# Optimization experiments

Hardware: AMD Instinct MI355X
Metric: run time of the kernel (lower is better)

Reference implementation:

```python
import jax, jax.numpy as jnp
from jax import lax
import numpy as np

CONF = 0.5        # config.video.detection_confidence
MAX_FACES = 8     # config.video.max_faces
EPS = 1e-5        # BatchNorm eps (inference mode: running stats)


def setup_inputs() -> dict:
    key = jax.random.key(0)
    ks = jax.random.split(key, 8)
    def w(k, shape):
        return jax.random.normal(k, shape, jnp.float32) * 0.05
    B, H, W = 32, 512, 512
    f32 = jnp.float32
    return {
        "x": jax.random.normal(ks[0], (B, 3, H, W), f32),
        # backbone conv1 (3->32, s2) + BN
        "w1": w(ks[1], (32, 3, 3, 3)), "b1": jnp.zeros(32, f32),
        "g1": jnp.ones(32, f32), "be1": jnp.zeros(32, f32),
        "m1": jnp.zeros(32, f32), "v1": jnp.ones(32, f32),
        # backbone conv2 (32->64, s2) + BN
        "w2": w(ks[2], (64, 32, 3, 3)), "b2": jnp.zeros(64, f32),
        "g2": jnp.ones(64, f32), "be2": jnp.zeros(64, f32),
        "m2": jnp.zeros(64, f32), "v2": jnp.ones(64, f32),
        # backbone conv3 (64->128, s2) + BN
        "w3": w(ks[3], (128, 64, 3, 3)), "b3": jnp.zeros(128, f32),
        "g3": jnp.ones(128, f32), "be3": jnp.zeros(128, f32),
        "m3": jnp.zeros(128, f32), "v3": jnp.ones(128, f32),
        # detection head (128->256 k3, 256->1 k1)
        "dw1": w(ks[4], (256, 128, 3, 3)), "db1": jnp.zeros(256, f32),
        "dw2": w(ks[5], (1, 256, 1, 1)), "db2": jnp.zeros(1, f32),
        # bbox head (128->256 k3, 256->4 k1)
        "bw1": w(ks[6], (256, 128, 3, 3)), "bb1": jnp.zeros(256, f32),
        "bw2": w(ks[7], (4, 256, 1, 1)), "bb2": jnp.zeros(4, f32),
    }


def _conv(x, w, b, stride, pad):
    y = lax.conv_general_dilated(x, w, (stride, stride), ((pad, pad), (pad, pad)),
                                 dimension_numbers=("NCHW", "OIHW", "NCHW"))
    return y + b[None, :, None, None]


def _bn(x, g, b, m, v):
    scale = (g * lax.rsqrt(v + EPS))[None, :, None, None]
    return (x - m[None, :, None, None]) * scale + b[None, :, None, None]


def reference(x, w1, b1, g1, be1, m1, v1, w2, b2, g2, be2, m2, v2,
              w3, b3, g3, be3, m3, v3, dw1, db1, dw2, db2, bw1, bb1, bw2, bb2):
    h = jax.nn.relu(_bn(_conv(x, w1, b1, 2, 1), g1, be1, m1, v1))
    h = jax.nn.relu(_bn(_conv(h, w2, b2, 2, 1), g2, be2, m2, v2))
    h = jax.nn.relu(_bn(_conv(h, w3, b3, 2, 1), g3, be3, m3, v3))
    # heads
    det = jax.nn.sigmoid(_conv(jax.nn.relu(_conv(h, dw1, db1, 1, 1)), dw2, db2, 1, 0))[:, 0]  # [B,Hf,Wf]
    bbox = _conv(jax.nn.relu(_conv(h, bw1, bb1, 1, 1)), bw2, bb2, 1, 0)  # [B,4,Hf,Wf]
    # fused threshold + top-k + gather (fixed-size, jit-friendly version of the per-image loop)
    B = det.shape[0]
    scores = det.reshape(B, -1)                      # [B, Hf*Wf]
    top_s, top_i = lax.top_k(scores, MAX_FACES)      # [B, K]
    bflat = bbox.reshape(B, 4, -1)                   # [B, 4, Hf*Wf]
    sel = jnp.take_along_axis(bflat, top_i[:, None, :], axis=2)  # [B, 4, K]
    boxes = jax.nn.sigmoid(jnp.swapaxes(sel, 1, 2)) * x.shape[-1]  # [B, K, 4]
    mask = (top_s > CONF)[:, :, None]                # below-threshold slots -> zeros
    return jnp.where(mask, boxes, jnp.zeros((), boxes.dtype))
```

## Files before the change

kernel.cpp:

```cpp
#include <hip/hip_runtime.h>
#include <math.h>

#define EPSBN 1e-5f

typedef __attribute__((ext_vector_type(4))) float f32x4;
typedef __attribute__((ext_vector_type(8))) short s16x8;

__device__ __forceinline__ unsigned short f2bf(float f) {
    unsigned u = __builtin_bit_cast(unsigned, f);
    u = (u + 0x7fffu + ((u >> 16) & 1u)) >> 16;
    return (unsigned short)u;
}
__device__ __forceinline__ float bf2f(unsigned short s) {
    unsigned u = ((unsigned)s) << 16;
    return __builtin_bit_cast(float, u);
}


__global__ __launch_bounds__(256) void prep_k(
    const float* __restrict__ w1, const float* __restrict__ b1, const float* __restrict__ g1,
    const float* __restrict__ be1, const float* __restrict__ m1, const float* __restrict__ v1,
    const float* __restrict__ w2, const float* __restrict__ b2, const float* __restrict__ g2,
    const float* __restrict__ be2, const float* __restrict__ m2, const float* __restrict__ v2,
    const float* __restrict__ w3, const float* __restrict__ b3, const float* __restrict__ g3,
    const float* __restrict__ be3, const float* __restrict__ m3, const float* __restrict__ v3,
    float* __restrict__ W)
{
    int i = blockIdx.x * 256 + threadIdx.x;
    if (i < 864) {
        int co = i & 31; int r = i >> 5; int ci = r % 3; int kk = r / 3;
        float A = g1[co] * rsqrtf(v1[co] + EPSBN);
        W[i] = w1[(co*3 + ci)*9 + kk] * A;
    } else if (i < 896) {
        int co = i - 864;
        float A = g1[co] * rsqrtf(v1[co] + EPSBN);
        W[i] = (b1[co] - m1[co]) * A + be1[co];
    } else if (i >= 19328 && i < 19392) {
        int co = i - 19328;
        float A = g2[co] * rsqrtf(v2[co] + EPSBN);
        W[i] = (b2[co] - m2[co]) * A + be2[co];
    } else if (i >= 93120 && i < 93248) {
        int co = i - 93120;
        float A = g3[co] * rsqrtf(v3[co] + EPSBN);
        W[i] = (b3[co] - m3[co]) * A + be3[co];
    }
}

__global__ __launch_bounds__(256) void prep2_k(
    const float* __restrict__ dw1, const float* __restrict__ bw1,
    unsigned short* __restrict__ WF)
{
    int i = blockIdx.x * 256 + threadIdx.x;
    if (i >= 1179648) return;
    int head = i / 589824;
    int r    = i - head * 589824;
    int kk   = r >> 16;
    int r2   = r & 65535;
    int cig  = r2 >> 14;
    int pl   = (r2 >> 13) & 1;
    int nf   = (r2 >> 9) & 15;
    int lane = (r2 >> 3) & 63;
    int j    = r2 & 7;
    int ci = cig*32 + (lane >> 4)*8 + j;
    int co = (lane & 15) + nf*16;
    const float* src = head ? bw1 : dw1;
    float w = src[(co*128 + ci)*9 + kk];
    unsigned short h = f2bf(w);
    WF[i] = pl ? f2bf(w - bf2f(h)) : h;
}

__global__ __launch_bounds__(256) void prep3_k(
    const float* __restrict__ w3, const float* __restrict__ g3, const float* __restrict__ v3,
    unsigned short* __restrict__ W3F)
{
    int i = blockIdx.x * 256 + threadIdx.x;
    if (i >= 147456) return;
    int kk = i >> 14;
    int r  = i & 16383;
    int cig = r >> 13;
    int pl  = (r >> 12) & 1;
    int nf  = (r >> 9) & 7;
    int lane = (r >> 3) & 63;
    int j   = r & 7;
    int ci = cig*32 + (lane >> 4)*8 + j;
    int co = nf*16 + (lane & 15);
    float A = g3[co] * rsqrtf(v3[co] + EPSBN);
    float w = w3[(co*64 + ci)*9 + kk] * A;
    unsigned short h = f2bf(w);
    W3F[i] = pl ? f2bf(w - bf2f(h)) : h;
}

__global__ __launch_bounds__(256) void prep4_k(
    const float* __restrict__ w2, const float* __restrict__ g2, const float* __restrict__ v2,
    unsigned short* __restrict__ W2F)
{
    int i = blockIdx.x * 256 + threadIdx.x;
    if (i >= 36864) return;
    int kk = i >> 12;
    int r  = i & 4095;
    int pl  = r >> 11;
    int nfg = (r >> 9) & 3;
    int lane = (r >> 3) & 63;
    int j   = r & 7;
    int ci = (lane >> 4)*8 + j;
    int co = nfg*16 + (lane & 15);
    float A = g2[co] * rsqrtf(v2[co] + EPSBN);
    float w = w2[(co*32 + ci)*9 + kk] * A;
    unsigned short h = f2bf(w);
    W2F[i] = pl ? f2bf(w - bf2f(h)) : h;
}

__global__ __launch_bounds__(256, 4) void conv12mm_k(
    const float* __restrict__ x, const float* __restrict__ W,
    const unsigned short* __restrict__ W2F,
    unsigned short* __restrict__ A2H, unsigned short* __restrict__ A2L, int b0)
{
    __shared__ __attribute__((aligned(16))) unsigned short Ah[9792];
    __shared__ __attribute__((aligned(16))) unsigned short Al[9792];

    const int tid  = threadIdx.x;
    const int lane = tid & 63;
    const int wv   = tid >> 6;
    const int m    = lane & 15;
    const int ks   = lane >> 4;

    const int bl   = blockIdx.x >> 8;
    const int tile = blockIdx.x & 255;
    const int OY = (tile >> 3) * 4;
    const int OX = (tile & 7) * 16;
    const int base1y = 2*OY - 1, base1x = 2*OX - 1;

    const float* xb = x + (size_t)(b0 + bl) * 3 * 262144;

    for (int t = tid; t < 297; t += 256) {
        int row = t / 33, lx = t - row*33;
        int y1 = base1y + row, x1 = base1x + lx;
        float c1[32];
        #pragma unroll
        for (int c = 0; c < 32; c++) c1[c] = 0.f;
        if (((unsigned)y1 < 256u) && ((unsigned)x1 < 256u)) {
            #pragma unroll
            for (int ky = 0; ky < 3; ky++) {
                int xy = 2*y1 + ky - 1;
                if ((unsigned)xy < 512u) {
                    #pragma unroll
                    for (int kx = 0; kx < 3; kx++) {
                        int xx = 2*x1 + kx - 1;
                        if ((unsigned)xx < 512u) {
                            int kk = ky*3 + kx;
                            #pragma unroll
                            for (int ci = 0; ci < 3; ci++) {
                                float v = xb[(size_t)ci*262144 + xy*512 + xx];
                                const float4* w4 = (const float4*)(W + (kk*3+ci)*32);
                                float4 wa = w4[0], wb = w4[1], wc = w4[2], wd = w4[3];
                                float4 we = w4[4], wf = w4[5], wg = w4[6], wh = w4[7];
                                c1[0]  = fmaf(v, wa.x, c1[0]);  c1[1]  = fmaf(v, wa.y, c1[1]);
                                c1[2]  = fmaf(v, wa.z, c1[2]);  c1[3]  = fmaf(v, wa.w, c1[3]);
                                c1[4]  = fmaf(v, wb.x, c1[4]);  c1[5]  = fmaf(v, wb.y, c1[5]);
                                c1[6]  = fmaf(v, wb.z, c1[6]);  c1[7]  = fmaf(v, wb.w, c1[7]);
                                c1[8]  = fmaf(v, wc.x, c1[8]);  c1[9]  = fmaf(v, wc.y, c1[9]);
                                c1[10] = fmaf(v, wc.z, c1[10]); c1[11] = fmaf(v, wc.w, c1[11]);
                                c1[12] = fmaf(v, wd.x, c1[12]); c1[13] = fmaf(v, wd.y, c1[13]);
                                c1[14] = fmaf(v, wd.z, c1[14]); c1[15] = fmaf(v, wd.w, c1[15]);
                                c1[16] = fmaf(v, we.x, c1[16]); c1[17] = fmaf(v, we.y, c1[17]);
                                c1[18] = fmaf(v, we.z, c1[18]); c1[19] = fmaf(v, we.w, c1[19]);
                                c1[20] = fmaf(v, wf.x, c1[20]); c1[21] = fmaf(v, wf.y, c1[21]);
                                c1[22] = fmaf(v, wf.z, c1[22]); c1[23] = fmaf(v, wf.w, c1[23]);
                                c1[24] = fmaf(v, wg.x, c1[24]); c1[25] = fmaf(v, wg.y, c1[25]);
                                c1[26] = fmaf(v, wg.z, c1[26]); c1[27] = fmaf(v, wg.w, c1[27]);
                                c1[28] = fmaf(v, wh.x, c1[28]); c1[29] = fmaf(v, wh.y, c1[29]);
                                c1[30] = fmaf(v, wh.z, c1[30]); c1[31] = fmaf(v, wh.w, c1[31]);
                            }
                        }
                    }
                }
            }
            #pragma unroll
            for (int c = 0; c < 32; c++)
                c1[c] = fmaxf(c1[c] + W[864 + c], 0.f);
        }
        int xi = (lx & 1)*17 + (lx >> 1);
        #pragma unroll
        for (int kg = 0; kg < 4; kg++) {
            uint4 h, l;
            unsigned hw[4], lw[4];
            #pragma unroll
            for (int q = 0; q < 4; q++) {
                float r0 = c1[kg*8 + 2*q], r1 = c1[kg*8 + 2*q + 1];
                unsigned short h0 = f2bf(r0), h1 = f2bf(r1);
                unsigned short l0 = f2bf(r0 - bf2f(h0)), l1 = f2bf(r1 - bf2f(h1));
                hw[q] = (unsigned)h0 | ((unsigned)h1 << 16);
                lw[q] = (unsigned)l0 | ((unsigned)l1 << 16);
            }
            h.x = hw[0]; h.y = hw[1]; h.z = hw[2]; h.w = hw[3];
            l.x = lw[0]; l.y = lw[1]; l.z = lw[2]; l.w = lw[3];
            int a = ((kg*9 + row)*34 + xi)*8;
            *(uint4*)&Ah[a] = h;
            *(uint4*)&Al[a] = l;
        }
    }
    __syncthreads();

    f32x4 acc[4];
    #pragma unroll
    for (int mf = 0; mf < 4; mf++) { f32x4 z = {0.f,0.f,0.f,0.f}; acc[mf] = z; }

    for (int ky = 0; ky < 3; ky++) {
        for (int kx = 0; kx < 3; kx++) {
            int kk = ky*3 + kx;
            int xib = (kx & 1)*17 + (kx >> 1);
            s16x8 ah[4], al[4];
            #pragma unroll
            for (int mf = 0; mf < 4; mf++) {
                int hy = 2*mf + ky;
                int a = ((ks*9 + hy)*34 + xib + m)*8;
                ah[mf] = *(const s16x8*)&Ah[a];
                al[mf] = *(const s16x8*)&Al[a];
            }
            const unsigned short* wb = W2F + kk*4096;
            s16x8 bh  = *(const s16x8*)(wb + wv*512 + lane*8);
            s16x8 blo = *(const s16x8*)(wb + 2048 + wv*512 + lane*8);
            #pragma unroll
            for (int mf = 0; mf < 4; mf++) {
                acc[mf] = __builtin_amdgcn_mfma_f32_16x16x32_bf16(ah[mf], bh,  acc[mf], 0, 0, 0);
                acc[mf] = __builtin_amdgcn_mfma_f32_16x16x32_bf16(ah[mf], blo, acc[mf], 0, 0, 0);
                acc[mf] = __builtin_amdgcn_mfma_f32_16x16x32_bf16(al[mf], bh,  acc[mf], 0, 0, 0);
            }
        }
    }

    const int co = wv*16 + m;
    const float bv = W[19328 + co];
    #pragma unroll
    for (int mf = 0; mf < 4; mf++) {
        int y = OY + mf;
        #pragma unroll
        for (int r = 0; r < 4; r++) {
            int xo = OX + ks*4 + r;
            float rv = fmaxf(acc[mf][r] + bv, 0.f);
            unsigned short h = f2bf(rv);
            unsigned short l = f2bf(rv - bf2f(h));
            size_t a = ((size_t)(bl*16384 + y*128 + xo))*64 + co;
            A2H[a] = h;
            A2L[a] = l;
        }
    }
}

__global__ __launch_bounds__(256, 2) void conv3mm_k(
    const unsigned short* __restrict__ A2H, const unsigned short* __restrict__ A2L,
    const unsigned short* __restrict__ W3F, const float* __restrict__ bias,
    unsigned* __restrict__ A3P)
{
    const int tid  = threadIdx.x;
    const int lane = tid & 63;
    const int w    = tid >> 6;
    const int bl   = blockIdx.x >> 6;
    const int y    = blockIdx.x & 63;
    const int m    = lane & 15;
    const int ks   = lane >> 4;

    f32x4 acc[4][2];
    #pragma unroll
    for (int mf = 0; mf < 4; mf++)
        #pragma unroll
        for (int nfl = 0; nfl < 2; nfl++) {
            f32x4 z = {0.f, 0.f, 0.f, 0.f};
            acc[mf][nfl] = z;
        }

    const size_t ibase = (size_t)bl * 16384 * 64;

    for (int ky = 0; ky < 3; ky++) {
        int iy = 2*y + ky - 1;
        if ((unsigned)iy >= 128u) continue;
        for (int kx = 0; kx < 3; kx++) {
            int kk = ky*3 + kx;
            #pragma unroll
            for (int cig = 0; cig < 2; cig++) {
                s16x8 ah[4], al[4];
                #pragma unroll
                for (int mf = 0; mf < 4; mf++) {
                    int xo = mf*16 + m;
                    int ix = 2*xo + kx - 1;
                    bool v = ix >= 0;
                    int ixc = v ? ix : 0;
                    size_t a = ibase + ((size_t)iy*128 + ixc)*64 + cig*32 + ks*8;
                    s16x8 zh = {0,0,0,0,0,0,0,0};
                    s16x8 th = *(const s16x8*)(A2H + a);
                    s16x8 tl = *(const s16x8*)(A2L + a);
                    ah[mf] = v ? th : zh;
                    al[mf] = v ? tl : zh;
                }
                const unsigned short* wb = W3F + (kk*2 + cig)*8192;
                #pragma unroll
                for (int nfl = 0; nfl < 2; nfl++) {
                    int nfg = w*2 + nfl;
                    s16x8 bh  = *(const s16x8*)(wb + nfg*512 + lane*8);
                    s16x8 blo = *(const s16x8*)(wb + 4096 + nfg*512 + lane*8);
                    #pragma unroll
                    for (int mf = 0; mf < 4; mf++) {
                        acc[mf][nfl] = __builtin_amdgcn_mfma_f32_16x16x32_bf16(ah[mf], bh,  acc[mf][nfl], 0, 0, 0);
                        acc[mf][nfl] = __builtin_amdgcn_mfma_f32_16x16x32_bf16(ah[mf], blo, acc[mf][nfl], 0, 0, 0);
                        acc[mf][nfl] = __builtin_amdgcn_mfma_f32_16x16x32_bf16(al[mf], bh,  acc[mf][nfl], 0, 0, 0);
                    }
                }
            }
        }
    }

    const size_t obase = ((size_t)(bl*64 + y))*64*128;
    #pragma unroll
    for (int nfl = 0; nfl < 2; nfl++) {
        int co = (w*2 + nfl)*16 + m;
        float bv = bias[co];
        #pragma unroll
        for (int mf = 0; mf < 4; mf++) {
            #pragma unroll
            for (int r = 0; r < 4; r++) {
                float rv = fmaxf(acc[mf][nfl][r] + bv, 0.f);
                unsigned short h = f2bf(rv);
                unsigned short l = f2bf(rv - bf2f(h));
                int xo = mf*16 + ks*4 + r;
                A3P[obase + (size_t)xo*128 + co] = (unsigned)h | ((unsigned)l << 16);
            }
        }
    }
}

__global__ __launch_bounds__(512, 4) void headmm_k(
    const unsigned* __restrict__ A3P, const unsigned short* __restrict__ WF,
    const float* __restrict__ db1, const float* __restrict__ dw2, const float* __restrict__ db2,
    const float* __restrict__ bb1, const float* __restrict__ bw2, const float* __restrict__ bb2,
    float* __restrict__ SC, float* __restrict__ BF, int b0)
{
    __shared__ __attribute__((aligned(16))) unsigned short Ah[6528];
    __shared__ __attribute__((aligned(16))) unsigned short Al[6528];
    __shared__ float red[8][4][64];

    const int tid  = threadIdx.x;
    const int lane = tid & 63;
    const int w    = tid >> 6;
    const int head = blockIdx.y;
    const int imgl = blockIdx.x >> 6;
    const int y    = blockIdx.x & 63;

    f32x4 acc[4][2];
    #pragma unroll
    for (int mf = 0; mf < 4; mf++)
        #pragma unroll
        for (int nf = 0; nf < 2; nf++) {
            f32x4 z = {0.f, 0.f, 0.f, 0.f};
            acc[mf][nf] = z;
        }

    const unsigned* abase = A3P + (size_t)imgl * 64 * 64 * 128;
    const unsigned short* WFh = WF + head * 589824;

    uint4 pva[2], pvb[2];
    #define HM_ISSUE(CIG)                                                          \
        _Pragma("unroll")                                                          \
        for (int it = 0; it < 2; it++) {                                           \
            int t = tid + it*512;                                                  \
            uint4 z4 = {0u,0u,0u,0u};                                              \
            pva[it] = z4; pvb[it] = z4;                                            \
            if (t < 792) {                                                         \
                int kgrp = t & 3; int q = t >> 2;                                  \
                int xi = q % 66;  int row = q / 66;                                \
                int gr = y + row - 1, gx = xi - 1;                                 \
                if (((unsigned)gr < 64u) && ((unsigned)gx < 64u)) {                \
                    const uint4* p = (const uint4*)(abase + ((size_t)gr*64 + gx)*128 \
                                                    + (CIG)*32 + kgrp*8);          \
                    pva[it] = p[0]; pvb[it] = p[1];                                \
                }                                                                  \
            }                                                                      \
        }

    HM_ISSUE(0);
    for (int cig = 0; cig < 4; cig++) {
        __syncthreads();
        #pragma unroll
        for (int it = 0; it < 2; it++) {
            int t = tid + it*512;
            if (t < 792) {
                int kgrp = t & 3; int q = t >> 2;
                int xi = q % 66;  int row = q / 66;
                int a = ((kgrp*3 + row)*68 + xi)*8;
                uint4 va = pva[it], vb = pvb[it];
                uint4 h, l;
                h.x = (va.x & 0xffffu) | (va.y << 16);
                h.y = (va.z & 0xffffu) | (va.w << 16);
                h.z = (vb.x & 0xffffu) | (vb.y << 16);
                h.w = (vb.z & 0xffffu) | (vb.w << 16);
                l.x = (va.x >> 16) | (va.y & 0xffff0000u);
                l.y = (va.z >> 16) | (va.w & 0xffff0000u);
                l.z = (vb.x >> 16) | (vb.y & 0xffff0000u);
                l.w = (vb.z >> 16) | (vb.w & 0xffff0000u);
                *(uint4*)&Ah[a] = h;
                *(uint4*)&Al[a] = l;
            }
        }
        if (cig < 3) { HM_ISSUE(cig + 1); }
        __syncthreads();
        __builtin_amdgcn_s_setprio(1);
        #pragma unroll 1
        for (int kk = 0; kk < 9; kk++) {
            int ky = kk / 3, kx = kk - 3*(kk/3);
            s16x8 ah[4], al[4];
            #pragma unroll
            for (int mf = 0; mf < 4; mf++) {
                int xq = (lane & 15) + 16*mf + kx;
                int a = (((lane >> 4)*3 + ky)*68 + xq)*8;
                ah[mf] = *(const s16x8*)&Ah[a];
                al[mf] = *(const s16x8*)&Al[a];
            }
            const unsigned short* wk = WFh + kk*65536 + cig*16384;
            #pragma unroll
            for (int nf = 0; nf < 2; nf++) {
                int nfg = w*2 + nf;
                s16x8 bh = *(const s16x8*)(wk + nfg*512 + lane*8);
                s16x8 bl = *(const s16x8*)(wk + 8192 + nfg*512 + lane*8);
                #pragma unroll
                for (int mf = 0; mf < 4; mf++) {
                    acc[mf][nf] = __builtin_amdgcn_mfma_f32_16x16x32_bf16(ah[mf], bh, acc[mf][nf], 0, 0, 0);
                    acc[mf][nf] = __builtin_amdgcn_mfma_f32_16x16x32_bf16(ah[mf], bl, acc[mf][nf], 0, 0, 0);
                    acc[mf][nf] = __builtin_amdgcn_mfma_f32_16x16x32_bf16(al[mf], bh, acc[mf][nf], 0, 0, 0);
                }
            }
        }
        __builtin_amdgcn_s_setprio(0);
    }
    #undef HM_ISSUE

    const float* b1p = head ? bb1 : db1;
    const float* w2p = head ? bw2 : dw2;
    const float* b2p = head ? bb2 : db2;
    const int NOUT = head ? 4 : 1;

    #pragma unroll
    for (int nf = 0; nf < 2; nf++) {
        float bv = b1p[(lane & 15) + (w*2 + nf)*16];
        #pragma unroll
        for (int mf = 0; mf < 4; mf++)
            #pragma unroll
            for (int r = 0; r < 4; r++)
                acc[mf][nf][r] = fmaxf(acc[mf][nf][r] + bv, 0.f);
    }

    for (int p = 0; p < NOUT; p++) {
        float wq0 = w2p[p*256 + (lane & 15) + (w*2 + 0)*16];
        float wq1 = w2p[p*256 + (lane & 15) + (w*2 + 1)*16];
        #pragma unroll
        for (int mf = 0; mf < 4; mf++) {
            #pragma unroll
            for (int r = 0; r < 4; r++) {
                float v = acc[mf][0][r]*wq0 + acc[mf][1][r]*wq1;
                v += __shfl_xor(v, 1);
                v += __shfl_xor(v, 2);
                v += __shfl_xor(v, 4);
                v += __shfl_xor(v, 8);
                if ((lane & 15) == 0)
                    red[w][p][mf*16 + (lane >> 4)*4 + r] = v;
            }
        }
    }
    __syncthreads();
    float* outp = head ? BF : SC;
    if (tid < NOUT*64) {
        int p = tid >> 6; int px = tid & 63;
        float v = b2p[p];
        #pragma unroll
        for (int ww = 0; ww < 8; ww++) v += red[ww][p][px];
        outp[((size_t)((b0 + imgl)*NOUT + p))*4096 + y*64 + px] = v;
    }
}

__global__ __launch_bounds__(256) void topk_k(
    const float* __restrict__ scores, const float* __restrict__ bflat,
    float* __restrict__ outp)
{
    __shared__ float sv[4096];
    __shared__ float rv[256];
    __shared__ int   ri[256];
    __shared__ float kv[8];
    __shared__ int   kidx[8];
    int b = blockIdx.x, t = threadIdx.x;
    for (int i = t; i < 4096; i += 256) sv[i] = scores[b*4096 + i];
    __syncthreads();
    for (int k = 0; k < 8; k++) {
        float bv = -INFINITY; int bi = 0x7fffffff;
        for (int i = t; i < 4096; i += 256) {
            float v = sv[i];
            if (v > bv || (v == bv && i < bi)) { bv = v; bi = i; }
        }
        rv[t] = bv; ri[t] = bi;
        __syncthreads();
        for (int s = 128; s > 0; s >>= 1) {
            if (t < s) {
                float v2 = rv[t+s]; int i2 = ri[t+s];
                if (v2 > rv[t] || (v2 == rv[t] && i2 < ri[t])) { rv[t] = v2; ri[t] = i2; }
            }
            __syncthreads();
        }
        if (t == 0) { kv[k] = rv[0]; kidx[k] = ri[0]; sv[ri[0]] = -INFINITY; }
        __syncthreads();
    }
    if (t < 32) {
        int k = t >> 2, c = t & 3;
        int idx = kidx[k];
        float s  = 1.f / (1.f + expf(-kv[k]));
        float lg = bflat[((size_t)(b*4 + c))*4096 + idx];
        float box = 512.f / (1.f + expf(-lg));
        outp[(b*8 + k)*4 + c] = (s > 0.5f) ? box : 0.f;
    }
}

extern "C" void kernel_launch(void* const* d_in, const int* in_sizes, int n_in,
                              void* d_out, int out_size, void* d_ws, size_t ws_size,
                              hipStream_t stream)
{
    const float* x   = (const float*)d_in[0];
    const float* w1  = (const float*)d_in[1];
    const float* b1  = (const float*)d_in[2];
    const float* g1  = (const float*)d_in[3];
    const float* be1 = (const float*)d_in[4];
    const float* m1  = (const float*)d_in[5];
    const float* v1  = (const float*)d_in[6];
    const float* w2  = (const float*)d_in[7];
    const float* b2  = (const float*)d_in[8];
    const float* g2  = (const float*)d_in[9];
    const float* be2 = (const float*)d_in[10];
    const float* m2  = (const float*)d_in[11];
    const float* v2  = (const float*)d_in[12];
    const float* w3  = (const float*)d_in[13];
    const float* b3  = (const float*)d_in[14];
    const float* g3  = (const float*)d_in[15];
    const float* be3 = (const float*)d_in[16];
    const float* m3  = (const float*)d_in[17];
    const float* v3  = (const float*)d_in[18];
    const float* dw1 = (const float*)d_in[19];
    const float* db1 = (const float*)d_in[20];
    const float* dw2 = (const float*)d_in[21];
    const float* db2 = (const float*)d_in[22];
    const float* bw1 = (const float*)d_in[23];
    const float* bb1 = (const float*)d_in[24];
    const float* bw2 = (const float*)d_in[25];
    const float* bb2 = (const float*)d_in[26];

    char*  wsb = (char*)d_ws;
    float*          W   = (float*)wsb;
    unsigned short* WF  = (unsigned short*)(wsb + 372992);
    unsigned short* W3F = (unsigned short*)(wsb + 2732288);
    float*          SC  = (float*)(wsb + 3027200);
    float*          BF  = (float*)(wsb + 3551488);
    unsigned short* A2H = (unsigned short*)(wsb + 5648640);
    unsigned short* A2L = (unsigned short*)(wsb + 22425856);
    unsigned*       A3P = (unsigned*)(wsb + 39203072);
    unsigned short* W2F = (unsigned short*)(wsb + 55980288);
    float* out = (float*)d_out;

    prep_k <<<365, 256, 0, stream>>>(w1,b1,g1,be1,m1,v1, w2,b2,g2,be2,m2,v2,
                                     w3,b3,g3,be3,m3,v3, W);
    prep2_k<<<4608, 256, 0, stream>>>(dw1, bw1, WF);
    prep3_k<<<576, 256, 0, stream>>>(w3, g3, v3, W3F);
    prep4_k<<<144, 256, 0, stream>>>(w2, g2, v2, W2F);

    for (int c = 0; c < 4; c++) {
        conv12mm_k<<<2048, 256, 0, stream>>>(x, W, W2F, A2H, A2L, c*8);
        conv3mm_k <<<512, 256, 0, stream>>>(A2H, A2L, W3F, W + 93120, A3P);
        headmm_k  <<<dim3(512, 2), 512, 0, stream>>>(A3P, WF, db1, dw2, db2, bb1, bw2, bb2,
                                                     SC, BF, c*8);
    }
    topk_k<<<32, 256, 0, stream>>>(SC, BF, out);
}
```

Baseline: 728.5 us.

## Fuse detection and bbox heads into one block to share staged activations

The head kernel now computes both heads in the same block instead of launching a separate grid row per head. The staged activation tile in shared memory and its global loads are reused for both weight sets, halving activation traffic and the split/convert work. In exchange, each thread holds twice the accumulators, launch bounds drop to 2 blocks per CU, and the grid has half as many blocks, lowering occupancy. The LDS row stride is also changed from 3 to 4 rows, which enlarges the shared buffers.

```diff
diff --git a/kernel.cpp b/kernel.cpp
--- a/kernel.cpp
+++ b/kernel.cpp
@@ -328,34 +328,34 @@
     }
 }
 
-__global__ __launch_bounds__(512, 4) void headmm_k(
+__global__ __launch_bounds__(512, 2) void headmm_k(
     const unsigned* __restrict__ A3P, const unsigned short* __restrict__ WF,
     const float* __restrict__ db1, const float* __restrict__ dw2, const float* __restrict__ db2,
     const float* __restrict__ bb1, const float* __restrict__ bw2, const float* __restrict__ bb2,
     float* __restrict__ SC, float* __restrict__ BF, int b0)
 {
-    __shared__ __attribute__((aligned(16))) unsigned short Ah[6528];
-    __shared__ __attribute__((aligned(16))) unsigned short Al[6528];
+    __shared__ __attribute__((aligned(16))) unsigned short Ah[8704];
+    __shared__ __attribute__((aligned(16))) unsigned short Al[8704];
     __shared__ float red[8][4][64];
 
     const int tid  = threadIdx.x;
     const int lane = tid & 63;
     const int w    = tid >> 6;
-    const int head = blockIdx.y;
     const int imgl = blockIdx.x >> 6;
     const int y    = blockIdx.x & 63;
 
-    f32x4 acc[4][2];
+    f32x4 acc[4][2][2];
     #pragma unroll
     for (int mf = 0; mf < 4; mf++)
         #pragma unroll
-        for (int nf = 0; nf < 2; nf++) {
-            f32x4 z = {0.f, 0.f, 0.f, 0.f};
-            acc[mf][nf] = z;
-        }
+        for (int nf = 0; nf < 2; nf++)
+            #pragma unroll
+            for (int h = 0; h < 2; h++) {
+                f32x4 z = {0.f, 0.f, 0.f, 0.f};
+                acc[mf][nf][h] = z;
+            }
 
     const unsigned* abase = A3P + (size_t)imgl * 64 * 64 * 128;
-    const unsigned short* WFh = WF + head * 589824;
 
     uint4 pva[2], pvb[2];
     #define HM_ISSUE(CIG)                                                          \
@@ -385,7 +385,7 @@
             if (t < 792) {
                 int kgrp = t & 3; int q = t >> 2;
                 int xi = q % 66;  int row = q / 66;
-                int a = ((kgrp*3 + row)*68 + xi)*8;
+                int a = ((kgrp*4 + row)*68 + xi)*8;
                 uint4 va = pva[it], vb = pvb[it];
                 uint4 h, l;
                 h.x = (va.x & 0xffffu) | (va.y << 16);
@@ -410,21 +410,24 @@
             #pragma unroll
             for (int mf = 0; mf < 4; mf++) {
                 int xq = (lane & 15) + 16*mf + kx;
-                int a = (((lane >> 4)*3 + ky)*68 + xq)*8;
+                int a = (((lane >> 4)*4 + ky)*68 + xq)*8;
                 ah[mf] = *(const s16x8*)&Ah[a];
                 al[mf] = *(const s16x8*)&Al[a];
             }
-            const unsigned short* wk = WFh + kk*65536 + cig*16384;
-            #pragma unroll
-            for (int nf = 0; nf < 2; nf++) {
-                int nfg = w*2 + nf;
-                s16x8 bh = *(const s16x8*)(wk + nfg*512 + lane*8);
-                s16x8 bl = *(const s16x8*)(wk + 8192 + nfg*512 + lane*8);
+            #pragma unroll
+            for (int h = 0; h < 2; h++) {
+                const unsigned short* wk = WF + h*589824 + kk*65536 + cig*16384;
                 #pragma unroll
-                for (int mf = 0; mf < 4; mf++) {
-                    acc[mf][nf] = __builtin_amdgcn_mfma_f32_16x16x32_bf16(ah[mf], bh, acc[mf][nf], 0, 0, 0);
-                    acc[mf][nf] = __builtin_amdgcn_mfma_f32_16x16x32_bf16(ah[mf], bl, acc[mf][nf], 0, 0, 0);
-                    acc[mf][nf] = __builtin_amdgcn_mfma_f32_16x16x32_bf16(al[mf], bh, acc[mf][nf], 0, 0, 0);
+                for (int nf = 0; nf < 2; nf++) {
+                    int nfg = w*2 + nf;
+                    s16x8 bh = *(const s16x8*)(wk + nfg*512 + lane*8);
+                    s16x8 bl = *(const s16x8*)(wk + 8192 + nfg*512 + lane*8);
+                    #pragma unroll
+                    for (int mf = 0; mf < 4; mf++) {
+                        acc[mf][nf][h] = __builtin_amdgcn_mfma_f32_16x16x32_bf16(ah[mf], bh, acc[mf][nf][h], 0, 0, 0);
+                        acc[mf][nf][h] = __builtin_amdgcn_mfma_f32_16x16x32_bf16(ah[mf], bl, acc[mf][nf][h], 0, 0, 0);
+                        acc[mf][nf][h] = __builtin_amdgcn_mfma_f32_16x16x32_bf16(al[mf], bh, acc[mf][nf][h], 0, 0, 0);
+                    }
                 }
             }
         }
@@ -432,46 +435,50 @@
     }
     #undef HM_ISSUE
 
-    const float* b1p = head ? bb1 : db1;
-    const float* w2p = head ? bw2 : dw2;
-    const float* b2p = head ? bb2 : db2;
-    const int NOUT = head ? 4 : 1;
-
-    #pragma unroll
-    for (int nf = 0; nf < 2; nf++) {
-        float bv = b1p[(lane & 15) + (w*2 + nf)*16];
-        #pragma unroll
-        for (int mf = 0; mf < 4; mf++)
-            #pragma unroll
-            for (int r = 0; r < 4; r++)
-                acc[mf][nf][r] = fmaxf(acc[mf][nf][r] + bv, 0.f);
-    }
-
-    for (int p = 0; p < NOUT; p++) {
-        float wq0 = w2p[p*256 + (lane & 15) + (w*2 + 0)*16];
-        float wq1 = w2p[p*256 + (lane & 15) + (w*2 + 1)*16];
-        #pragma unroll
-        for (int mf = 0; mf < 4; mf++) {
-            #pragma unroll
-            for (int r = 0; r < 4; r++) {
-                float v = acc[mf][0][r]*wq0 + acc[mf][1][r]*wq1;
-                v += __shfl_xor(v, 1);
-                v += __shfl_xor(v, 2);
-                v += __shfl_xor(v, 4);
-                v += __shfl_xor(v, 8);
-                if ((lane & 15) == 0)
-                    red[w][p][mf*16 + (lane >> 4)*4 + r] = v;
-            }
-        }
-    }
-    __syncthreads();
-    float* outp = head ? BF : SC;
-    if (tid < NOUT*64) {
-        int p = tid >> 6; int px = tid & 63;
-        float v = b2p[p];
-        #pragma unroll
-        for (int ww = 0; ww < 8; ww++) v += red[ww][p][px];
-        outp[((size_t)((b0 + imgl)*NOUT + p))*4096 + y*64 + px] = v;
+    #pragma unroll 1
+    for (int h = 0; h < 2; h++) {
+        const float* b1p = h ? bb1 : db1;
+        const float* w2p = h ? bw2 : dw2;
+        const float* b2p = h ? bb2 : db2;
+        const int NOUT = h ? 4 : 1;
+
+        #pragma unroll
+        for (int nf = 0; nf < 2; nf++) {
+            float bv = b1p[(lane & 15) + (w*2 + nf)*16];
+            #pragma unroll
+            for (int mf = 0; mf < 4; mf++)
+                #pragma unroll
+                for (int r = 0; r < 4; r++)
+                    acc[mf][nf][h][r] = fmaxf(acc[mf][nf][h][r] + bv, 0.f);
+        }
+
+        for (int p = 0; p < NOUT; p++) {
+            float wq0 = w2p[p*256 + (lane & 15) + (w*2 + 0)*16];
+            float wq1 = w2p[p*256 + (lane & 15) + (w*2 + 1)*16];
+            #pragma unroll
+            for (int mf = 0; mf < 4; mf++) {
+                #pragma unroll
+                for (int r = 0; r < 4; r++) {
+                    float v = acc[mf][0][h][r]*wq0 + acc[mf][1][h][r]*wq1;
+                    v += __shfl_xor(v, 1);
+                    v += __shfl_xor(v, 2);
+                    v += __shfl_xor(v, 4);
+                    v += __shfl_xor(v, 8);
+                    if ((lane & 15) == 0)
+                        red[w][p][mf*16 + (lane >> 4)*4 + r] = v;
+                }
+            }
+        }
+        __syncthreads();
+        float* outp = h ? BF : SC;
+        if (tid < NOUT*64) {
+            int p = tid >> 6; int px = tid & 63;
+            float v = b2p[p];
+            #pragma unroll
+            for (int ww = 0; ww < 8; ww++) v += red[ww][p][px];
+            outp[((size_t)((b0 + imgl)*NOUT + p))*4096 + y*64 + px] = v;
+        }
+        __syncthreads();
     }
 }
 
@@ -568,8 +575,8 @@
     for (int c = 0; c < 4; c++) {
         conv12mm_k<<<2048, 256, 0, stream>>>(x, W, W2F, A2H, A2L, c*8);
         conv3mm_k <<<512, 256, 0, stream>>>(A2H, A2L, W3F, W + 93120, A3P);
-        headmm_k  <<<dim3(512, 2), 512, 0, stream>>>(A3P, WF, db1, dw2, db2, bb1, bw2, bb2,
-                                                     SC, BF, c*8);
+        headmm_k  <<<512, 512, 0, stream>>>(A3P, WF, db1, dw2, db2, bb1, bw2, bb2,
+                                            SC, BF, c*8);
     }
     topk_k<<<32, 256, 0, stream>>>(SC, BF, out);
 }
```

After: 1.143 ms. 56.9% more time.
